# Optimization experiments

Measured on AMD Instinct MI355X. Metric: run time of the kernel, lower is better.

## Reference

```python
import jax, jax.numpy as jnp
import numpy as np

N = 50000      # nodes (full graph: num_dst == num_src == N)
E = 800000     # edges, avg degree 16
D = 128        # in_feats == n_hidden == out_feats
L = 3          # n_layers
EPS = 1e-5     # BatchNorm1d eps


def setup_inputs() -> dict:
    key = jax.random.key(0)
    ks = jax.random.split(key, 6)
    feat = jax.random.normal(ks[0], (N, D), dtype=jnp.float32)
    src = jax.random.randint(ks[1], (E,), 0, N)
    dst = jax.random.randint(ks[2], (E,), 0, N)
    scale = 1.0 / np.sqrt(D)
    W_self = jax.random.normal(ks[3], (L, D, D), dtype=jnp.float32) * scale
    W_neigh = jax.random.normal(ks[4], (L, D, D), dtype=jnp.float32) * scale
    b = jax.random.normal(ks[5], (L, D), dtype=jnp.float32) * 0.01
    gamma = jnp.ones((L - 1, D), dtype=jnp.float32)
    beta = jnp.zeros((L - 1, D), dtype=jnp.float32)
    return {"feat": feat, "src": src, "dst": dst, "W_self": W_self,
            "W_neigh": W_neigh, "b": b, "gamma": gamma, "beta": beta}


def reference(feat, src, dst, W_self, W_neigh, b, gamma, beta):
    n = feat.shape[0]
    n_layers = W_self.shape[0]
    # in-degree of each dst node, clamped to 1 (zero-degree nodes aggregate 0)
    deg = jax.ops.segment_sum(jnp.ones_like(dst, dtype=feat.dtype), dst,
                              num_segments=n)
    deg = jnp.maximum(deg, 1.0)[:, None]                      # [N,1]
    h = feat
    for i in range(n_layers):
        # mean aggregation over incoming neighbors: gather + segment-sum
        agg = jax.ops.segment_sum(h[src], dst, num_segments=n) / deg  # [N,D]
        # SAGEConv('mean'): fc_self(h_dst) + fc_neigh(agg) + bias
        hn = h @ W_self[i] + agg @ W_neigh[i] + b[i]
        hn = hn + h                                           # residual (dims match)
        if i < n_layers - 1:
            mu = jnp.mean(hn, axis=0)
            var = jnp.var(hn, axis=0)                         # biased, as BN training
            hn = (hn - mu) * jax.lax.rsqrt(var + EPS) * gamma[i] + beta[i]
            hn = jax.nn.relu(hn)
        h = hn
    return h
```

## Files before the change

kernel.cpp:

```cpp
#include <hip/hip_runtime.h>

#define DIM 128
#define EPSF 1e-5f
#define BK_SHIFT 8
#define BK_NODES 256
#define GRP_SHIFT 13
#define NGRP 8
#define BKS_CAP 1536
#define MAXNBS 1600

typedef __attribute__((ext_vector_type(8))) short short8;
typedef __attribute__((ext_vector_type(4))) float float4v;

__device__ inline unsigned short f2bf(float x) {
    union { float f; unsigned u; } z; z.f = x;
    unsigned u = z.u;
    unsigned r = u + 0x7FFF + ((u >> 16) & 1);
    return (unsigned short)(r >> 16);
}
__device__ inline float bf2f(unsigned short u) {
    union { unsigned u; float f; } z; z.u = ((unsigned)u) << 16;
    return z.f;
}

__global__ void binA_kernel(const int* __restrict__ src, const int* __restrict__ dst,
                            unsigned* __restrict__ barr, int* __restrict__ bcnt,
                            int E, int NBS) {
    __shared__ int cnt[MAXNBS];
    __shared__ int gcur[MAXNBS];
    int tid = threadIdx.x;
    int tile0 = blockIdx.x * 4096;
    for (int j = tid; j < NBS; j += 256) cnt[j] = 0;
    __syncthreads();
    unsigned pk[16]; int bk[16];
#pragma unroll
    for (int i = 0; i < 16; ++i) {
        int e = tile0 + i * 256 + tid;
        if (e < E) {
            int d = dst[e];
            int s = src[e];
            bk[i] = ((d >> BK_SHIFT) << 3) | (s >> GRP_SHIFT);
            pk[i] = ((unsigned)(d & (BK_NODES - 1)) << 16) | (unsigned)s;
            atomicAdd(&cnt[bk[i]], 1);
        } else bk[i] = -1;
    }
    __syncthreads();
    for (int j = tid; j < NBS; j += 256) {
        int c = cnt[j];
        gcur[j] = (c > 0) ? atomicAdd(&bcnt[j], c) : 0;
    }
    __syncthreads();
#pragma unroll
    for (int i = 0; i < 16; ++i) {
        if (bk[i] >= 0) {
            int pos = atomicAdd(&gcur[bk[i]], 1);
            if (pos < BKS_CAP)
                barr[(size_t)bk[i] * BKS_CAP + pos] = pk[i];
        }
    }
}

__global__ void binB_kernel(const unsigned* __restrict__ barr, const int* __restrict__ bcnt,
                            int* __restrict__ rowptr, int* __restrict__ colidx,
                            int N, int E, int NBS) {
    __shared__ int hist[256];
    __shared__ int sm[256];
    __shared__ int bc[NGRP];
    int b = blockIdx.x;
    int tid = threadIdx.x;
    int lim = b * NGRP;
    int part = 0;
    for (int i = tid; i < lim; i += 256) part += bcnt[i];
    sm[tid] = part;
    if (tid < NGRP) bc[tid] = bcnt[lim + tid];
    __syncthreads();
    for (int off = 128; off > 0; off >>= 1) {
        if (tid < off) sm[tid] += sm[tid + off];
        __syncthreads();
    }
    int gb = sm[0];
    if (b == 0 && tid == 0) rowptr[N] = E;
    __syncthreads();
    hist[tid] = 0;
    __syncthreads();
    for (int g = 0; g < NGRP; ++g) {
        int cg = bc[g]; if (cg > BKS_CAP) cg = BKS_CAP;
        const unsigned* arr = barr + (size_t)(b * NGRP + g) * BKS_CAP;
        for (int i = tid; i < cg; i += 256)
            atomicAdd(&hist[arr[i] >> 16], 1);
    }
    __syncthreads();
    int h = hist[tid];
    sm[tid] = h;
    __syncthreads();
    for (int off = 1; off < 256; off <<= 1) {
        int x = (tid >= off) ? sm[tid - off] : 0;
        __syncthreads();
        sm[tid] += x;
        __syncthreads();
    }
    int base = sm[tid] - h;
    hist[tid] = base;
    int node = (b << BK_SHIFT) + tid;
    if (node < N) rowptr[node] = gb + base;
    __syncthreads();
    for (int g = 0; g < NGRP; ++g) {
        int cg = bc[g]; if (cg > BKS_CAP) cg = BKS_CAP;
        const unsigned* arr = barr + (size_t)(b * NGRP + g) * BKS_CAP;
        for (int i = tid; i < cg; i += 256) {
            unsigned u = arr[i];
            int pos = atomicAdd(&hist[u >> 16], 1);
            colidx[gb + pos] = (int)(u & 0xFFFFu);
        }
        __syncthreads();
    }
}

__global__ void packw_kernel(const float* __restrict__ Ws, const float* __restrict__ Wn,
                             unsigned short* __restrict__ wpack) {
    int l = blockIdx.x >> 3;
    int s = blockIdx.x & 7;
    int tid = threadIdx.x;
#pragma unroll
    for (int pi = 0; pi < 2; ++pi) {
        int p = tid * 2 + pi;
        int nt = p >> 6;
        int lane = p & 63;
        int kb = s * 32 + (lane >> 4) * 8;
        int col = nt * 16 + (lane & 15);
        unsigned short* dstp = wpack + (size_t)l * 32768 + ((size_t)(s * 8 + nt) * 64 + lane) * 8;
#pragma unroll
        for (int j = 0; j < 8; ++j) {
            int k = kb + j;
            float v = (k < 128) ? Ws[(size_t)l * 16384 + k * 128 + col]
                                : Wn[(size_t)l * 16384 + (k - 128) * 128 + col];
            dstp[j] = f2bf(v);
        }
    }
}

__global__ void convert_kernel(const float* __restrict__ feat, unsigned short* __restrict__ Acat,
                               int N) {
    int idx = blockIdx.x * blockDim.x + threadIdx.x;
    if (idx >= N * 32) return;
    float4 v = ((const float4*)feat)[idx];
    int r = idx >> 5, c4 = idx & 31;
    ushort4 o;
    o.x = f2bf(v.x); o.y = f2bf(v.y); o.z = f2bf(v.z); o.w = f2bf(v.w);
    ((ushort4*)Acat)[(size_t)r * 64 + c4] = o;
}

__global__ void aggregate_kernel(unsigned short* Acat, const int* __restrict__ rowptr,
                                 const int* __restrict__ colidx, float* __restrict__ stats,
                                 int N) {
    if (blockIdx.x == 0) stats[threadIdx.x] = 0.f;
    int wid = (blockIdx.x * blockDim.x + threadIdx.x) >> 6;
    if (wid >= N) return;
    int lane = threadIdx.x & 63;
    int half = lane >> 5, sl = lane & 31;
    int beg = rowptr[wid], end = rowptr[wid + 1];
    float4 acc = make_float4(0.f, 0.f, 0.f, 0.f);
    int e = beg + half;
    for (; e + 6 < end; e += 8) {
        int s0 = colidx[e];
        int s1 = colidx[e + 2];
        int s2 = colidx[e + 4];
        int s3 = colidx[e + 6];
        ushort4 u0 = *(const ushort4*)(Acat + (size_t)s0 * 256 + sl * 4);
        ushort4 u1 = *(const ushort4*)(Acat + (size_t)s1 * 256 + sl * 4);
        ushort4 u2 = *(const ushort4*)(Acat + (size_t)s2 * 256 + sl * 4);
        ushort4 u3 = *(const ushort4*)(Acat + (size_t)s3 * 256 + sl * 4);
        acc.x += (bf2f(u0.x) + bf2f(u1.x)) + (bf2f(u2.x) + bf2f(u3.x));
        acc.y += (bf2f(u0.y) + bf2f(u1.y)) + (bf2f(u2.y) + bf2f(u3.y));
        acc.z += (bf2f(u0.z) + bf2f(u1.z)) + (bf2f(u2.z) + bf2f(u3.z));
        acc.w += (bf2f(u0.w) + bf2f(u1.w)) + (bf2f(u2.w) + bf2f(u3.w));
    }
    for (; e < end; e += 2) {
        int s0 = colidx[e];
        ushort4 u0 = *(const ushort4*)(Acat + (size_t)s0 * 256 + sl * 4);
        acc.x += bf2f(u0.x);
        acc.y += bf2f(u0.y);
        acc.z += bf2f(u0.z);
        acc.w += bf2f(u0.w);
    }
    acc.x += __shfl_xor(acc.x, 32);
    acc.y += __shfl_xor(acc.y, 32);
    acc.z += __shfl_xor(acc.z, 32);
    acc.w += __shfl_xor(acc.w, 32);
    if (half == 0) {
        int deg = end - beg;
        float inv = 1.0f / (float)(deg > 0 ? deg : 1);
        ushort4 o;
        o.x = f2bf(acc.x * inv); o.y = f2bf(acc.y * inv);
        o.z = f2bf(acc.z * inv); o.w = f2bf(acc.w * inv);
        *(ushort4*)(Acat + (size_t)wid * 256 + 128 + sl * 4) = o;
    }
}

__launch_bounds__(256)
__global__ void gemm_kernel(const unsigned short* __restrict__ Acat,
                            const unsigned short* __restrict__ wpack,
                            const float* __restrict__ bias,
                            unsigned short* __restrict__ outb, float* __restrict__ outf,
                            float* __restrict__ stats, int withStats, int N) {
    __shared__ unsigned short Bs[32768];
    int tid = threadIdx.x;
    {
        const float4* wsrc = (const float4*)wpack;
        float4* bdst = (float4*)Bs;
#pragma unroll
        for (int i = 0; i < 16; ++i) bdst[i * 256 + tid] = wsrc[i * 256 + tid];
    }
    __syncthreads();

    int wave = tid >> 6, lane = tid & 63;
    int row0 = blockIdx.x * 128 + wave * 32;
    int mrow = lane & 15, kq = lane >> 4;
    const unsigned short* Abase = Acat + (size_t)(row0 + mrow) * 256 + kq * 8;

    float4v acc[2][8];
#pragma unroll
    for (int i = 0; i < 2; ++i)
#pragma unroll
        for (int j = 0; j < 8; ++j) acc[i][j] = (float4v){0.f, 0.f, 0.f, 0.f};

#pragma unroll
    for (int s = 0; s < 8; ++s) {
        short8 a0 = *(const short8*)(Abase + s * 32);
        short8 a1 = *(const short8*)(Abase + 16 * 256 + s * 32);
#pragma unroll
        for (int nt = 0; nt < 8; ++nt) {
            short8 b = *(const short8*)(Bs + ((size_t)(s * 8 + nt) * 64 + lane) * 8);
            acc[0][nt] = __builtin_amdgcn_mfma_f32_16x16x32_bf16(a0, b, acc[0][nt], 0, 0, 0);
            acc[1][nt] = __builtin_amdgcn_mfma_f32_16x16x32_bf16(a1, b, acc[1][nt], 0, 0, 0);
        }
    }

    float* sm = (float*)Bs;
    if (withStats) {
        __syncthreads();
        sm[tid] = 0.f;
        __syncthreads();
    }

    int colb = lane & 15;
    int rq = (lane >> 4) * 4;
#pragma unroll
    for (int mt = 0; mt < 2; ++mt) {
        int rowt = row0 + mt * 16 + rq;
#pragma unroll
        for (int nt = 0; nt < 8; ++nt) {
            int col = nt * 16 + colb;
            float bv = bias[col];
            float slo = 0.f, qlo = 0.f;
#pragma unroll
            for (int r = 0; r < 4; ++r) {
                int row = rowt + r;
                if (row < N) {
                    float res = bf2f(Acat[(size_t)row * 256 + col]);
                    float v = acc[mt][nt][r] + bv + res;
                    if (withStats) {
                        outb[(size_t)row * 128 + col] = f2bf(v);
                        slo += v; qlo += v * v;
                    } else {
                        outf[(size_t)row * 128 + col] = v;
                    }
                }
            }
            if (withStats) {
                atomicAdd(&sm[col], slo);
                atomicAdd(&sm[128 + col], qlo);
            }
        }
    }
    if (withStats) {
        __syncthreads();
        if (tid < 128) {
            atomicAdd(&stats[tid], sm[tid]);
            atomicAdd(&stats[128 + tid], sm[128 + tid]);
        }
    }
}

__global__ void bnapply_kernel(const unsigned short* __restrict__ hn,
                               unsigned short* __restrict__ Acat,
                               const float* __restrict__ stats, const float* __restrict__ gamma,
                               const float* __restrict__ beta, float invN, int N) {
    __shared__ float sc_s[128], sh_s[128];
    int tid = threadIdx.x;
    if (tid < 128) {
        float mean = stats[tid] * invN;
        float var = stats[128 + tid] * invN - mean * mean;
        float sc = gamma[tid] * rsqrtf(var + EPSF);
        sc_s[tid] = sc;
        sh_s[tid] = beta[tid] - mean * sc;
    }
    __syncthreads();
    int idx = blockIdx.x * 256 + tid;
    if (idx >= N * 32) return;
    int row = idx >> 5, c4 = idx & 31;
    ushort4 u = *(const ushort4*)(hn + (size_t)idx * 4);
    ushort4 o;
    {
        int col = c4 * 4;
        float v0 = fmaf(bf2f(u.x), sc_s[col], sh_s[col]);
        float v1 = fmaf(bf2f(u.y), sc_s[col + 1], sh_s[col + 1]);
        float v2 = fmaf(bf2f(u.z), sc_s[col + 2], sh_s[col + 2]);
        float v3 = fmaf(bf2f(u.w), sc_s[col + 3], sh_s[col + 3]);
        o.x = f2bf(fmaxf(v0, 0.f));
        o.y = f2bf(fmaxf(v1, 0.f));
        o.z = f2bf(fmaxf(v2, 0.f));
        o.w = f2bf(fmaxf(v3, 0.f));
    }
    *(ushort4*)(Acat + (size_t)row * 256 + c4 * 4) = o;
}

extern "C" void kernel_launch(void* const* d_in, const int* in_sizes, int n_in,
                              void* d_out, int out_size, void* d_ws, size_t ws_size,
                              hipStream_t stream) {
    const float* feat  = (const float*)d_in[0];
    const int*   src   = (const int*)d_in[1];
    const int*   dst   = (const int*)d_in[2];
    const float* Wself = (const float*)d_in[3];
    const float* Wneig = (const float*)d_in[4];
    const float* bias  = (const float*)d_in[5];
    const float* gamma = (const float*)d_in[6];
    const float* beta  = (const float*)d_in[7];

    int N = in_sizes[0] / DIM;
    int E = in_sizes[1];
    int Npad = (N + 127) & ~127;
    int NB = (N + BK_NODES - 1) >> BK_SHIFT;
    int NBS = NB * NGRP;

    char* ws = (char*)d_ws;
    size_t off = 0;
    auto alloc = [&](size_t bytes) -> void* {
        void* p = ws + off;
        off = (off + bytes + 255) & ~(size_t)255;
        return p;
    };
    unsigned short* Acat   = (unsigned short*)alloc((size_t)Npad * 256 * 2);
    unsigned short* hnS    = (unsigned short*)alloc((size_t)Npad * 128 * 2);
    unsigned short* wpack  = (unsigned short*)alloc((size_t)3 * 32768 * 2);
    int*   colidx = (int*)alloc((size_t)E * 4);
    int*   rowptr = (int*)alloc((size_t)(N + 1) * 4);
    int*   bcnt   = (int*)alloc(MAXNBS * 4);
    float* stats  = (float*)alloc(256 * 4);

    unsigned* barr = (unsigned*)Acat;

    hipMemsetAsync(bcnt, 0, MAXNBS * 4, stream);
    binA_kernel<<<(E + 4095) / 4096, 256, 0, stream>>>(src, dst, barr, bcnt, E, NBS);
    binB_kernel<<<NB, 256, 0, stream>>>(barr, bcnt, rowptr, colidx, N, E, NBS);

    packw_kernel<<<24, 256, 0, stream>>>(Wself, Wneig, wpack);
    convert_kernel<<<(N * 32 + 255) / 256, 256, 0, stream>>>(feat, Acat, N);
    if (Npad > N)
        hipMemsetAsync(Acat + (size_t)N * 256, 0, (size_t)(Npad - N) * 512, stream);

    float invN = 1.0f / (float)N;

    for (int l = 0; l < 3; ++l) {
        aggregate_kernel<<<(N + 3) / 4, 256, 0, stream>>>(Acat, rowptr, colidx, stats, N);
        int withStats = (l < 2) ? 1 : 0;
        gemm_kernel<<<Npad / 128, 256, 0, stream>>>(
            Acat, wpack + (size_t)l * 32768, bias + (size_t)l * DIM,
            hnS, (float*)d_out, stats, withStats, N);
        if (withStats)
            bnapply_kernel<<<(N * 32 + 255) / 256, 256, 0, stream>>>(
                hnS, Acat, stats, gamma + (size_t)l * DIM, beta + (size_t)l * DIM, invN, N);
    }
}
```

Before: 335.9 us.

## Fuse BatchNorm+ReLU into neighbor aggregation and merge prep kernels

Removes the separate bnapply pass. Aggregation now gathers from a compact N×128 bf16 hidden buffer and applies BN scale/shift plus ReLU to each gathered neighbor row on the fly. It also writes the normalized self row into the concatenated GEMM input. Weight packing and feature conversion are merged into one launch, and stats buffers are double-buffered and zeroed by the existing memset. This trades a full read/write pass per layer for extra FMA/max work per gathered edge, and it halves gather row stride, which may improve cache locality.

```diff
diff --git a/kernel.cpp b/kernel.cpp
--- a/kernel.cpp
+++ b/kernel.cpp
@@ -116,48 +116,69 @@
     }
 }
 
-__global__ void packw_kernel(const float* __restrict__ Ws, const float* __restrict__ Wn,
-                             unsigned short* __restrict__ wpack) {
-    int l = blockIdx.x >> 3;
-    int s = blockIdx.x & 7;
+__global__ void prep_kernel(const float* __restrict__ Ws, const float* __restrict__ Wn,
+                            unsigned short* __restrict__ wpack,
+                            const float* __restrict__ feat, unsigned short* __restrict__ Hd,
+                            int N) {
+    int b = blockIdx.x;
     int tid = threadIdx.x;
-#pragma unroll
-    for (int pi = 0; pi < 2; ++pi) {
-        int p = tid * 2 + pi;
-        int nt = p >> 6;
-        int lane = p & 63;
-        int kb = s * 32 + (lane >> 4) * 8;
-        int col = nt * 16 + (lane & 15);
-        unsigned short* dstp = wpack + (size_t)l * 32768 + ((size_t)(s * 8 + nt) * 64 + lane) * 8;
-#pragma unroll
-        for (int j = 0; j < 8; ++j) {
-            int k = kb + j;
-            float v = (k < 128) ? Ws[(size_t)l * 16384 + k * 128 + col]
-                                : Wn[(size_t)l * 16384 + (k - 128) * 128 + col];
-            dstp[j] = f2bf(v);
-        }
-    }
-}
-
-__global__ void convert_kernel(const float* __restrict__ feat, unsigned short* __restrict__ Acat,
-                               int N) {
-    int idx = blockIdx.x * blockDim.x + threadIdx.x;
+    if (b < 24) {
+        int l = b >> 3;
+        int s = b & 7;
+#pragma unroll
+        for (int pi = 0; pi < 2; ++pi) {
+            int p = tid * 2 + pi;
+            int nt = p >> 6;
+            int lane = p & 63;
+            int kb = s * 32 + (lane >> 4) * 8;
+            int col = nt * 16 + (lane & 15);
+            unsigned short* dstp = wpack + (size_t)l * 32768 + ((size_t)(s * 8 + nt) * 64 + lane) * 8;
+#pragma unroll
+            for (int j = 0; j < 8; ++j) {
+                int k = kb + j;
+                float v = (k < 128) ? Ws[(size_t)l * 16384 + k * 128 + col]
+                                    : Wn[(size_t)l * 16384 + (k - 128) * 128 + col];
+                dstp[j] = f2bf(v);
+            }
+        }
+        return;
+    }
+    int idx = (b - 24) * 256 + tid;
     if (idx >= N * 32) return;
     float4 v = ((const float4*)feat)[idx];
-    int r = idx >> 5, c4 = idx & 31;
     ushort4 o;
     o.x = f2bf(v.x); o.y = f2bf(v.y); o.z = f2bf(v.z); o.w = f2bf(v.w);
-    ((ushort4*)Acat)[(size_t)r * 64 + c4] = o;
-}
-
-__global__ void aggregate_kernel(unsigned short* Acat, const int* __restrict__ rowptr,
-                                 const int* __restrict__ colidx, float* __restrict__ stats,
-                                 int N) {
-    if (blockIdx.x == 0) stats[threadIdx.x] = 0.f;
+    ((ushort4*)Hd)[idx] = o;
+}
+
+template<int BN>
+__global__ void aggregate_kernel(const unsigned short* __restrict__ Hd,
+                                 unsigned short* __restrict__ Acat,
+                                 const int* __restrict__ rowptr,
+                                 const int* __restrict__ colidx,
+                                 const float* __restrict__ stats,
+                                 const float* __restrict__ gamma,
+                                 const float* __restrict__ beta,
+                                 float invN, int N) {
     int wid = (blockIdx.x * blockDim.x + threadIdx.x) >> 6;
     if (wid >= N) return;
     int lane = threadIdx.x & 63;
     int half = lane >> 5, sl = lane & 31;
+    float sc[4], sh[4];
+    if (BN) {
+#pragma unroll
+        for (int j = 0; j < 4; ++j) {
+            int c = sl * 4 + j;
+            float mean = stats[c] * invN;
+            float var = stats[128 + c] * invN - mean * mean;
+            float s = gamma[c] * rsqrtf(var + EPSF);
+            sc[j] = s; sh[j] = beta[c] - mean * s;
+        }
+    }
+#define BNOP0(x) fmaxf(fmaf(bf2f(x), sc[0], sh[0]), 0.f)
+#define BNOP1(x) fmaxf(fmaf(bf2f(x), sc[1], sh[1]), 0.f)
+#define BNOP2(x) fmaxf(fmaf(bf2f(x), sc[2], sh[2]), 0.f)
+#define BNOP3(x) fmaxf(fmaf(bf2f(x), sc[3], sh[3]), 0.f)
     int beg = rowptr[wid], end = rowptr[wid + 1];
     float4 acc = make_float4(0.f, 0.f, 0.f, 0.f);
     int e = beg + half;
@@ -166,22 +187,36 @@
         int s1 = colidx[e + 2];
         int s2 = colidx[e + 4];
         int s3 = colidx[e + 6];
-        ushort4 u0 = *(const ushort4*)(Acat + (size_t)s0 * 256 + sl * 4);
-        ushort4 u1 = *(const ushort4*)(Acat + (size_t)s1 * 256 + sl * 4);
-        ushort4 u2 = *(const ushort4*)(Acat + (size_t)s2 * 256 + sl * 4);
-        ushort4 u3 = *(const ushort4*)(Acat + (size_t)s3 * 256 + sl * 4);
-        acc.x += (bf2f(u0.x) + bf2f(u1.x)) + (bf2f(u2.x) + bf2f(u3.x));
-        acc.y += (bf2f(u0.y) + bf2f(u1.y)) + (bf2f(u2.y) + bf2f(u3.y));
-        acc.z += (bf2f(u0.z) + bf2f(u1.z)) + (bf2f(u2.z) + bf2f(u3.z));
-        acc.w += (bf2f(u0.w) + bf2f(u1.w)) + (bf2f(u2.w) + bf2f(u3.w));
+        ushort4 u0 = *(const ushort4*)(Hd + (size_t)s0 * 128 + sl * 4);
+        ushort4 u1 = *(const ushort4*)(Hd + (size_t)s1 * 128 + sl * 4);
+        ushort4 u2 = *(const ushort4*)(Hd + (size_t)s2 * 128 + sl * 4);
+        ushort4 u3 = *(const ushort4*)(Hd + (size_t)s3 * 128 + sl * 4);
+        if (BN) {
+            acc.x += (BNOP0(u0.x) + BNOP0(u1.x)) + (BNOP0(u2.x) + BNOP0(u3.x));
+            acc.y += (BNOP1(u0.y) + BNOP1(u1.y)) + (BNOP1(u2.y) + BNOP1(u3.y));
+            acc.z += (BNOP2(u0.z) + BNOP2(u1.z)) + (BNOP2(u2.z) + BNOP2(u3.z));
+            acc.w += (BNOP3(u0.w) + BNOP3(u1.w)) + (BNOP3(u2.w) + BNOP3(u3.w));
+        } else {
+            acc.x += (bf2f(u0.x) + bf2f(u1.x)) + (bf2f(u2.x) + bf2f(u3.x));
+            acc.y += (bf2f(u0.y) + bf2f(u1.y)) + (bf2f(u2.y) + bf2f(u3.y));
+            acc.z += (bf2f(u0.z) + bf2f(u1.z)) + (bf2f(u2.z) + bf2f(u3.z));
+            acc.w += (bf2f(u0.w) + bf2f(u1.w)) + (bf2f(u2.w) + bf2f(u3.w));
+        }
     }
     for (; e < end; e += 2) {
         int s0 = colidx[e];
-        ushort4 u0 = *(const ushort4*)(Acat + (size_t)s0 * 256 + sl * 4);
-        acc.x += bf2f(u0.x);
-        acc.y += bf2f(u0.y);
-        acc.z += bf2f(u0.z);
-        acc.w += bf2f(u0.w);
+        ushort4 u0 = *(const ushort4*)(Hd + (size_t)s0 * 128 + sl * 4);
+        if (BN) {
+            acc.x += BNOP0(u0.x);
+            acc.y += BNOP1(u0.y);
+            acc.z += BNOP2(u0.z);
+            acc.w += BNOP3(u0.w);
+        } else {
+            acc.x += bf2f(u0.x);
+            acc.y += bf2f(u0.y);
+            acc.z += bf2f(u0.z);
+            acc.w += bf2f(u0.w);
+        }
     }
     acc.x += __shfl_xor(acc.x, 32);
     acc.y += __shfl_xor(acc.y, 32);
@@ -190,11 +225,24 @@
     if (half == 0) {
         int deg = end - beg;
         float inv = 1.0f / (float)(deg > 0 ? deg : 1);
+        ushort4 hrow = *(const ushort4*)(Hd + (size_t)wid * 128 + sl * 4);
+        ushort4 ho;
+        if (BN) {
+            ho.x = f2bf(BNOP0(hrow.x));
+            ho.y = f2bf(BNOP1(hrow.y));
+            ho.z = f2bf(BNOP2(hrow.z));
+            ho.w = f2bf(BNOP3(hrow.w));
+        } else ho = hrow;
+        *(ushort4*)(Acat + (size_t)wid * 256 + sl * 4) = ho;
         ushort4 o;
         o.x = f2bf(acc.x * inv); o.y = f2bf(acc.y * inv);
         o.z = f2bf(acc.z * inv); o.w = f2bf(acc.w * inv);
         *(ushort4*)(Acat + (size_t)wid * 256 + 128 + sl * 4) = o;
     }
+#undef BNOP0
+#undef BNOP1
+#undef BNOP2
+#undef BNOP3
 }
 
 __launch_bounds__(256)
@@ -282,39 +330,6 @@
     }
 }
 
-__global__ void bnapply_kernel(const unsigned short* __restrict__ hn,
-                               unsigned short* __restrict__ Acat,
-                               const float* __restrict__ stats, const float* __restrict__ gamma,
-                               const float* __restrict__ beta, float invN, int N) {
-    __shared__ float sc_s[128], sh_s[128];
-    int tid = threadIdx.x;
-    if (tid < 128) {
-        float mean = stats[tid] * invN;
-        float var = stats[128 + tid] * invN - mean * mean;
-        float sc = gamma[tid] * rsqrtf(var + EPSF);
-        sc_s[tid] = sc;
-        sh_s[tid] = beta[tid] - mean * sc;
-    }
-    __syncthreads();
-    int idx = blockIdx.x * 256 + tid;
-    if (idx >= N * 32) return;
-    int row = idx >> 5, c4 = idx & 31;
-    ushort4 u = *(const ushort4*)(hn + (size_t)idx * 4);
-    ushort4 o;
-    {
-        int col = c4 * 4;
-        float v0 = fmaf(bf2f(u.x), sc_s[col], sh_s[col]);
-        float v1 = fmaf(bf2f(u.y), sc_s[col + 1], sh_s[col + 1]);
-        float v2 = fmaf(bf2f(u.z), sc_s[col + 2], sh_s[col + 2]);
-        float v3 = fmaf(bf2f(u.w), sc_s[col + 3], sh_s[col + 3]);
-        o.x = f2bf(fmaxf(v0, 0.f));
-        o.y = f2bf(fmaxf(v1, 0.f));
-        o.z = f2bf(fmaxf(v2, 0.f));
-        o.w = f2bf(fmaxf(v3, 0.f));
-    }
-    *(ushort4*)(Acat + (size_t)row * 256 + c4 * 4) = o;
-}
-
 extern "C" void kernel_launch(void* const* d_in, const int* in_sizes, int n_in,
                               void* d_out, int out_size, void* d_ws, size_t ws_size,
                               hipStream_t stream) {
@@ -341,34 +356,34 @@
         return p;
     };
     unsigned short* Acat   = (unsigned short*)alloc((size_t)Npad * 256 * 2);
-    unsigned short* hnS    = (unsigned short*)alloc((size_t)Npad * 128 * 2);
+    unsigned short* Hd     = (unsigned short*)alloc((size_t)Npad * 128 * 2);
     unsigned short* wpack  = (unsigned short*)alloc((size_t)3 * 32768 * 2);
     int*   colidx = (int*)alloc((size_t)E * 4);
     int*   rowptr = (int*)alloc((size_t)(N + 1) * 4);
     int*   bcnt   = (int*)alloc(MAXNBS * 4);
-    float* stats  = (float*)alloc(256 * 4);
+    float* stats  = (float*)alloc(512 * 4);
 
     unsigned* barr = (unsigned*)Acat;
 
-    hipMemsetAsync(bcnt, 0, MAXNBS * 4, stream);
+    hipMemsetAsync(bcnt, 0, MAXNBS * 4 + 512 * 4, stream);
     binA_kernel<<<(E + 4095) / 4096, 256, 0, stream>>>(src, dst, barr, bcnt, E, NBS);
     binB_kernel<<<NB, 256, 0, stream>>>(barr, bcnt, rowptr, colidx, N, E, NBS);
 
-    packw_kernel<<<24, 256, 0, stream>>>(Wself, Wneig, wpack);
-    convert_kernel<<<(N * 32 + 255) / 256, 256, 0, stream>>>(feat, Acat, N);
-    if (Npad > N)
-        hipMemsetAsync(Acat + (size_t)N * 256, 0, (size_t)(Npad - N) * 512, stream);
+    prep_kernel<<<24 + (N * 32 + 255) / 256, 256, 0, stream>>>(Wself, Wneig, wpack, feat, Hd, N);
 
     float invN = 1.0f / (float)N;
-
-    for (int l = 0; l < 3; ++l) {
-        aggregate_kernel<<<(N + 3) / 4, 256, 0, stream>>>(Acat, rowptr, colidx, stats, N);
-        int withStats = (l < 2) ? 1 : 0;
-        gemm_kernel<<<Npad / 128, 256, 0, stream>>>(
-            Acat, wpack + (size_t)l * 32768, bias + (size_t)l * DIM,
-            hnS, (float*)d_out, stats, withStats, N);
-        if (withStats)
-            bnapply_kernel<<<(N * 32 + 255) / 256, 256, 0, stream>>>(
-                hnS, Acat, stats, gamma + (size_t)l * DIM, beta + (size_t)l * DIM, invN, N);
-    }
-}
+    int nagg = (N + 3) / 4;
+
+    aggregate_kernel<0><<<nagg, 256, 0, stream>>>(Hd, Acat, rowptr, colidx,
+                                                  stats, gamma, beta, invN, N);
+    gemm_kernel<<<Npad / 128, 256, 0, stream>>>(Acat, wpack, bias, Hd, (float*)d_out,
+                                                stats, 1, N);
+    aggregate_kernel<1><<<nagg, 256, 0, stream>>>(Hd, Acat, rowptr, colidx,
+                                                  stats, gamma, beta, invN, N);
+    gemm_kernel<<<Npad / 128, 256, 0, stream>>>(Acat, wpack + 32768, bias + DIM, Hd,
+                                                (float*)d_out, stats + 256, 1, N);
+    aggregate_kernel<1><<<nagg, 256, 0, stream>>>(Hd, Acat, rowptr, colidx,
+                                                  stats + 256, gamma + DIM, beta + DIM, invN, N);
+    gemm_kernel<<<Npad / 128, 256, 0, stream>>>(Acat, wpack + 2 * 32768, bias + 2 * DIM, Hd,
+                                                (float*)d_out, stats, 0, N);
+}
```

Result: faster. 325.5 us (-3.1%).

## Split concatenated feature buffer into separate H and Agg arrays; fuse prep launches

Applied to the files above, without the earlier changes.

Replaces the interleaved [H | Agg] row buffer with separate contiguous H, Agg and pre-BN buffers. Neighbor gathers in aggregation now read densely packed 256-byte rows, so the gathered working set is smaller and more cache-friendly. The GEMM reads its two K-halves from the two buffers. Weight packing, feature conversion and the zeroing of bin counters and stats are merged into one prep kernel, which removes the memset calls. The loop is unrolled so each layer uses its own stats slot. Zeroing stats relies on the stats buffer sitting directly after the bin counters in the workspace, and padding rows are no longer zeroed.

```diff
diff --git a/kernel.cpp b/kernel.cpp
--- a/kernel.cpp
+++ b/kernel.cpp
@@ -116,44 +116,49 @@
     }
 }
 
-__global__ void packw_kernel(const float* __restrict__ Ws, const float* __restrict__ Wn,
-                             unsigned short* __restrict__ wpack) {
-    int l = blockIdx.x >> 3;
-    int s = blockIdx.x & 7;
-    int tid = threadIdx.x;
-#pragma unroll
-    for (int pi = 0; pi < 2; ++pi) {
-        int p = tid * 2 + pi;
-        int nt = p >> 6;
-        int lane = p & 63;
-        int kb = s * 32 + (lane >> 4) * 8;
-        int col = nt * 16 + (lane & 15);
-        unsigned short* dstp = wpack + (size_t)l * 32768 + ((size_t)(s * 8 + nt) * 64 + lane) * 8;
-#pragma unroll
-        for (int j = 0; j < 8; ++j) {
-            int k = kb + j;
-            float v = (k < 128) ? Ws[(size_t)l * 16384 + k * 128 + col]
-                                : Wn[(size_t)l * 16384 + (k - 128) * 128 + col];
-            dstp[j] = f2bf(v);
-        }
-    }
-}
-
-__global__ void convert_kernel(const float* __restrict__ feat, unsigned short* __restrict__ Acat,
-                               int N) {
-    int idx = blockIdx.x * blockDim.x + threadIdx.x;
+__global__ void prep_kernel(const float* __restrict__ Ws, const float* __restrict__ Wn,
+                            unsigned short* __restrict__ wpack,
+                            const float* __restrict__ feat, unsigned short* __restrict__ Hb,
+                            int* __restrict__ zbase, int N) {
+    int b = blockIdx.x;
+    int tid = threadIdx.x;
+    if (b < 24) {
+        int l = b >> 3;
+        int s = b & 7;
+#pragma unroll
+        for (int pi = 0; pi < 2; ++pi) {
+            int p = tid * 2 + pi;
+            int nt = p >> 6;
+            int lane = p & 63;
+            int kb = s * 32 + (lane >> 4) * 8;
+            int col = nt * 16 + (lane & 15);
+            unsigned short* dstp = wpack + (size_t)l * 32768 + ((size_t)(s * 8 + nt) * 64 + lane) * 8;
+#pragma unroll
+            for (int j = 0; j < 8; ++j) {
+                int k = kb + j;
+                float v = (k < 128) ? Ws[(size_t)l * 16384 + k * 128 + col]
+                                    : Wn[(size_t)l * 16384 + (k - 128) * 128 + col];
+                dstp[j] = f2bf(v);
+            }
+        }
+        return;
+    }
+    if (b == 24) {
+        for (int j = tid; j < MAXNBS + 512; j += 256) zbase[j] = 0;
+        return;
+    }
+    int idx = (b - 25) * 256 + tid;
     if (idx >= N * 32) return;
     float4 v = ((const float4*)feat)[idx];
-    int r = idx >> 5, c4 = idx & 31;
     ushort4 o;
     o.x = f2bf(v.x); o.y = f2bf(v.y); o.z = f2bf(v.z); o.w = f2bf(v.w);
-    ((ushort4*)Acat)[(size_t)r * 64 + c4] = o;
-}
-
-__global__ void aggregate_kernel(unsigned short* Acat, const int* __restrict__ rowptr,
-                                 const int* __restrict__ colidx, float* __restrict__ stats,
-                                 int N) {
-    if (blockIdx.x == 0) stats[threadIdx.x] = 0.f;
+    ((ushort4*)Hb)[idx] = o;
+}
+
+__global__ void aggregate_kernel(const unsigned short* __restrict__ Hb,
+                                 unsigned short* __restrict__ Agg,
+                                 const int* __restrict__ rowptr,
+                                 const int* __restrict__ colidx, int N) {
     int wid = (blockIdx.x * blockDim.x + threadIdx.x) >> 6;
     if (wid >= N) return;
     int lane = threadIdx.x & 63;
@@ -166,10 +171,10 @@
         int s1 = colidx[e + 2];
         int s2 = colidx[e + 4];
         int s3 = colidx[e + 6];
-        ushort4 u0 = *(const ushort4*)(Acat + (size_t)s0 * 256 + sl * 4);
-        ushort4 u1 = *(const ushort4*)(Acat + (size_t)s1 * 256 + sl * 4);
-        ushort4 u2 = *(const ushort4*)(Acat + (size_t)s2 * 256 + sl * 4);
-        ushort4 u3 = *(const ushort4*)(Acat + (size_t)s3 * 256 + sl * 4);
+        ushort4 u0 = *(const ushort4*)(Hb + (size_t)s0 * 128 + sl * 4);
+        ushort4 u1 = *(const ushort4*)(Hb + (size_t)s1 * 128 + sl * 4);
+        ushort4 u2 = *(const ushort4*)(Hb + (size_t)s2 * 128 + sl * 4);
+        ushort4 u3 = *(const ushort4*)(Hb + (size_t)s3 * 128 + sl * 4);
         acc.x += (bf2f(u0.x) + bf2f(u1.x)) + (bf2f(u2.x) + bf2f(u3.x));
         acc.y += (bf2f(u0.y) + bf2f(u1.y)) + (bf2f(u2.y) + bf2f(u3.y));
         acc.z += (bf2f(u0.z) + bf2f(u1.z)) + (bf2f(u2.z) + bf2f(u3.z));
@@ -177,7 +182,7 @@
     }
     for (; e < end; e += 2) {
         int s0 = colidx[e];
-        ushort4 u0 = *(const ushort4*)(Acat + (size_t)s0 * 256 + sl * 4);
+        ushort4 u0 = *(const ushort4*)(Hb + (size_t)s0 * 128 + sl * 4);
         acc.x += bf2f(u0.x);
         acc.y += bf2f(u0.y);
         acc.z += bf2f(u0.z);
@@ -193,12 +198,13 @@
         ushort4 o;
         o.x = f2bf(acc.x * inv); o.y = f2bf(acc.y * inv);
         o.z = f2bf(acc.z * inv); o.w = f2bf(acc.w * inv);
-        *(ushort4*)(Acat + (size_t)wid * 256 + 128 + sl * 4) = o;
+        *(ushort4*)(Agg + (size_t)wid * 128 + sl * 4) = o;
     }
 }
 
 __launch_bounds__(256)
-__global__ void gemm_kernel(const unsigned short* __restrict__ Acat,
+__global__ void gemm_kernel(const unsigned short* __restrict__ Hb,
+                            const unsigned short* __restrict__ Agg,
                             const unsigned short* __restrict__ wpack,
                             const float* __restrict__ bias,
                             unsigned short* __restrict__ outb, float* __restrict__ outf,
@@ -216,7 +222,8 @@
     int wave = tid >> 6, lane = tid & 63;
     int row0 = blockIdx.x * 128 + wave * 32;
     int mrow = lane & 15, kq = lane >> 4;
-    const unsigned short* Abase = Acat + (size_t)(row0 + mrow) * 256 + kq * 8;
+    const unsigned short* Sbase = Hb + (size_t)(row0 + mrow) * 128 + kq * 8;
+    const unsigned short* Gbase = Agg + (size_t)(row0 + mrow) * 128 + kq * 8;
 
     float4v acc[2][8];
 #pragma unroll
@@ -226,8 +233,9 @@
 
 #pragma unroll
     for (int s = 0; s < 8; ++s) {
-        short8 a0 = *(const short8*)(Abase + s * 32);
-        short8 a1 = *(const short8*)(Abase + 16 * 256 + s * 32);
+        const unsigned short* ab = (s < 4) ? (Sbase + s * 32) : (Gbase + (s - 4) * 32);
+        short8 a0 = *(const short8*)ab;
+        short8 a1 = *(const short8*)(ab + 16 * 128);
 #pragma unroll
         for (int nt = 0; nt < 8; ++nt) {
             short8 b = *(const short8*)(Bs + ((size_t)(s * 8 + nt) * 64 + lane) * 8);
@@ -257,7 +265,7 @@
             for (int r = 0; r < 4; ++r) {
                 int row = rowt + r;
                 if (row < N) {
-                    float res = bf2f(Acat[(size_t)row * 256 + col]);
+                    float res = bf2f(Hb[(size_t)row * 128 + col]);
                     float v = acc[mt][nt][r] + bv + res;
                     if (withStats) {
                         outb[(size_t)row * 128 + col] = f2bf(v);
@@ -282,10 +290,10 @@
     }
 }
 
-__global__ void bnapply_kernel(const unsigned short* __restrict__ hn,
-                               unsigned short* __restrict__ Acat,
-                               const float* __restrict__ stats, const float* __restrict__ gamma,
-                               const float* __restrict__ beta, float invN, int N) {
+__global__ void bn_kernel(const unsigned short* __restrict__ hn,
+                          unsigned short* __restrict__ Hb,
+                          const float* __restrict__ stats, const float* __restrict__ gamma,
+                          const float* __restrict__ beta, float invN, int N) {
     __shared__ float sc_s[128], sh_s[128];
     int tid = threadIdx.x;
     if (tid < 128) {
@@ -298,7 +306,7 @@
     __syncthreads();
     int idx = blockIdx.x * 256 + tid;
     if (idx >= N * 32) return;
-    int row = idx >> 5, c4 = idx & 31;
+    int c4 = idx & 31;
     ushort4 u = *(const ushort4*)(hn + (size_t)idx * 4);
     ushort4 o;
     {
@@ -312,7 +320,7 @@
         o.z = f2bf(fmaxf(v2, 0.f));
         o.w = f2bf(fmaxf(v3, 0.f));
     }
-    *(ushort4*)(Acat + (size_t)row * 256 + c4 * 4) = o;
+    *(ushort4*)(Hb + (size_t)idx * 4) = o;
 }
 
 extern "C" void kernel_launch(void* const* d_in, const int* in_sizes, int n_in,
@@ -340,35 +348,34 @@
         off = (off + bytes + 255) & ~(size_t)255;
         return p;
     };
-    unsigned short* Acat   = (unsigned short*)alloc((size_t)Npad * 256 * 2);
-    unsigned short* hnS    = (unsigned short*)alloc((size_t)Npad * 128 * 2);
-    unsigned short* wpack  = (unsigned short*)alloc((size_t)3 * 32768 * 2);
+    unsigned short* Hb    = (unsigned short*)alloc((size_t)Npad * 128 * 2);
+    unsigned short* Agg   = (unsigned short*)alloc((size_t)Npad * 128 * 2);
+    unsigned short* Hd    = (unsigned short*)alloc((size_t)Npad * 128 * 2);
+    unsigned short* wpack = (unsigned short*)alloc((size_t)3 * 32768 * 2);
     int*   colidx = (int*)alloc((size_t)E * 4);
     int*   rowptr = (int*)alloc((size_t)(N + 1) * 4);
     int*   bcnt   = (int*)alloc(MAXNBS * 4);
-    float* stats  = (float*)alloc(256 * 4);
-
-    unsigned* barr = (unsigned*)Acat;
-
-    hipMemsetAsync(bcnt, 0, MAXNBS * 4, stream);
+    float* stats  = (float*)alloc(512 * 4);
+
+    unsigned* barr = (unsigned*)Agg;
+
+    float invN = 1.0f / (float)N;
+    int nagg = (N + 3) / 4;
+    int nbn  = (N * 32 + 255) / 256;
+
+    prep_kernel<<<25 + nbn, 256, 0, stream>>>(Wself, Wneig, wpack, feat, Hb, bcnt, N);
     binA_kernel<<<(E + 4095) / 4096, 256, 0, stream>>>(src, dst, barr, bcnt, E, NBS);
     binB_kernel<<<NB, 256, 0, stream>>>(barr, bcnt, rowptr, colidx, N, E, NBS);
 
-    packw_kernel<<<24, 256, 0, stream>>>(Wself, Wneig, wpack);
-    convert_kernel<<<(N * 32 + 255) / 256, 256, 0, stream>>>(feat, Acat, N);
-    if (Npad > N)
-        hipMemsetAsync(Acat + (size_t)N * 256, 0, (size_t)(Npad - N) * 512, stream);
-
-    float invN = 1.0f / (float)N;
-
-    for (int l = 0; l < 3; ++l) {
-        aggregate_kernel<<<(N + 3) / 4, 256, 0, stream>>>(Acat, rowptr, colidx, stats, N);
-        int withStats = (l < 2) ? 1 : 0;
-        gemm_kernel<<<Npad / 128, 256, 0, stream>>>(
-            Acat, wpack + (size_t)l * 32768, bias + (size_t)l * DIM,
-            hnS, (float*)d_out, stats, withStats, N);
-        if (withStats)
-            bnapply_kernel<<<(N * 32 + 255) / 256, 256, 0, stream>>>(
-                hnS, Acat, stats, gamma + (size_t)l * DIM, beta + (size_t)l * DIM, invN, N);
-    }
-}
+    aggregate_kernel<<<nagg, 256, 0, stream>>>(Hb, Agg, rowptr, colidx, N);
+    gemm_kernel<<<Npad / 128, 256, 0, stream>>>(Hb, Agg, wpack, bias,
+                                                Hd, (float*)d_out, stats, 1, N);
+    bn_kernel<<<nbn, 256, 0, stream>>>(Hd, Hb, stats, gamma, beta, invN, N);
+    aggregate_kernel<<<nagg, 256, 0, stream>>>(Hb, Agg, rowptr, colidx, N);
+    gemm_kernel<<<Npad / 128, 256, 0, stream>>>(Hb, Agg, wpack + 32768, bias + DIM,
+                                                Hd, (float*)d_out, stats + 256, 1, N);
+    bn_kernel<<<nbn, 256, 0, stream>>>(Hd, Hb, stats + 256, gamma + DIM, beta + DIM, invN, N);
+    aggregate_kernel<<<nagg, 256, 0, stream>>>(Hb, Agg, rowptr, colidx, N);
+    gemm_kernel<<<Npad / 128, 256, 0, stream>>>(Hb, Agg, wpack + 2 * 32768, bias + 2 * DIM,
+                                                Hd, (float*)d_out, stats, 0, N);
+}
```

Measured after the change: 333.3 us. No clear change (-0.8%).
